# Performance work log

Measured on AMD Instinct MI355X. Metric: run time of the kernel, lower is better.

## Reference

```python
import jax, jax.numpy as jnp
import numpy as np

N_NODES = 50000
E0, E1 = 500000, 300000
D = 64  # node_embedding_size == h_feats == edge_embedding_sizes[i]


def _mlp(x, w0, b0, w1, b1, w2, b2):
    # Linear -> ReLU -> Linear -> ReLU -> Linear (nodes_in / edges_in stacks)
    h = jax.nn.relu(x @ w0 + b0)
    h = jax.nn.relu(h @ w1 + b1)
    return h @ w2 + b2


def setup_inputs() -> dict:
    key = jax.random.key(0)
    ks = jax.random.split(key, 32)

    def lin(k, fi, fo):
        return (jax.random.uniform(k, (fi, fo), jnp.float32) - 0.5) * (2.0 / np.sqrt(fi))

    z = lambda n: jnp.zeros((n,), jnp.float32)
    inp = {}
    inp['node_feats'] = jax.random.normal(ks[0], (N_NODES, 32), jnp.float32)
    inp['edge_feats0'] = jax.random.normal(ks[1], (E0, 16), jnp.float32)
    inp['edge_feats1'] = jax.random.normal(ks[2], (E1, 8), jnp.float32)
    # nodes_in MLP
    inp['n_w0'], inp['n_b0'] = lin(ks[3], 32, D), z(D)
    inp['n_w1'], inp['n_b1'] = lin(ks[4], D, D), z(D)
    inp['n_w2'], inp['n_b2'] = lin(ks[5], D, D), z(D)
    # edges_in MLP for edge type 0 (16 -> 64)
    inp['e0_w0'], inp['e0_b0'] = lin(ks[6], 16, D), z(D)
    inp['e0_w1'], inp['e0_b1'] = lin(ks[7], D, D), z(D)
    inp['e0_w2'], inp['e0_b2'] = lin(ks[8], D, D), z(D)
    # edges_in MLP for edge type 1 (8 -> 64)
    inp['e1_w0'], inp['e1_b0'] = lin(ks[9], 8, D), z(D)
    inp['e1_w1'], inp['e1_b1'] = lin(ks[10], D, D), z(D)
    inp['e1_w2'], inp['e1_b2'] = lin(ks[11], D, D), z(D)
    # GraphConv weights
    inp['c1_w'], inp['c1_b'] = lin(ks[12], D, D), z(D)
    inp['c2_w'], inp['c2_b'] = lin(ks[13], D, 1), z(1)
    # edge list (type-0 edges first, then type-1 edges)
    inp['src'] = jax.random.randint(ks[14], (E0 + E1,), 0, N_NODES, dtype=jnp.int32)
    inp['dst'] = jax.random.randint(ks[15], (E0 + E1,), 0, N_NODES, dtype=jnp.int32)
    return inp


def reference(node_feats, edge_feats0, edge_feats1,
              n_w0, n_b0, n_w1, n_b1, n_w2, n_b2,
              e0_w0, e0_b0, e0_w1, e0_b1, e0_w2, e0_b2,
              e1_w0, e1_b0, e1_w1, e1_b1, e1_w2, e1_b2,
              c1_w, c1_b, c2_w, c2_b, src, dst):
    n = node_feats.shape[0]
    # dense embedding stacks
    hn = _mlp(node_feats, n_w0, n_b0, n_w1, n_b1, n_w2, n_b2)          # [N, D]
    he = jnp.concatenate([
        _mlp(edge_feats0, e0_w0, e0_b0, e0_w1, e0_b1, e0_w2, e0_b2),
        _mlp(edge_feats1, e1_w0, e1_b0, e1_w1, e1_b1, e1_w2, e1_b2),
    ], axis=0)                                                          # [E, D]
    # GraphConv symmetric normalization (DGL norm='both'), degrees clamped to 1
    ones = jnp.ones(src.shape, jnp.float32)
    deg_out = jnp.maximum(jax.ops.segment_sum(ones, src, num_segments=n), 1.0)
    deg_in = jnp.maximum(jax.ops.segment_sum(ones, dst, num_segments=n), 1.0)
    norm_e = jax.lax.rsqrt(deg_out[src] * deg_in[dst])[:, None]        # [E, 1]
    # conv1: u_add_v message plus edge embedding, normalized sum aggregation
    msg = (hn[src] + hn[dst] + he) * norm_e                            # [E, D]
    agg1 = jax.ops.segment_sum(msg, dst, num_segments=n)               # [N, D]
    h1 = jax.nn.relu(agg1 @ c1_w + c1_b)                               # [N, D]
    # conv2: standard GraphConv to scalar output
    agg2 = jax.ops.segment_sum(h1[src] * norm_e, dst, num_segments=n)  # [N, D]
    return agg2 @ c2_w + c2_b                                          # [N, 1]
```

## Files before the change

### kernel.cpp

```cpp
#include <hip/hip_runtime.h>

#define N_NODES 50000
#define NE0 500000
#define NE1 300000
#define NE (NE0 + NE1)
#define DD 64

typedef __bf16 bf16x8 __attribute__((ext_vector_type(8)));
typedef float f32x4 __attribute__((ext_vector_type(4)));
typedef unsigned short u16x8 __attribute__((ext_vector_type(8)));

__device__ __forceinline__ ushort f2bf(float x) {
  union { __bf16 h; ushort u; } v;
  v.h = (__bf16)x;
  return v.u;
}
__device__ __forceinline__ float bf2f(ushort u) {
  union { unsigned u; float f; } v;
  v.u = ((unsigned)u) << 16;
  return v.f;
}

__device__ __forceinline__ int RP(const int* __restrict__ rowptr,
                                  const int* __restrict__ boff, int i) {
  return (i >= N_NODES) ? NE : rowptr[i] + boff[i >> 8];
}

__global__ void pack_k(const float* __restrict__ w00, const float* __restrict__ w01,
                       const float* __restrict__ w02, const float* __restrict__ w10,
                       const float* __restrict__ w11, const float* __restrict__ w12,
                       const float* __restrict__ w20, const float* __restrict__ w21,
                       const float* __restrict__ w22, ushort* __restrict__ pk) {
  int f = blockIdx.x, l = threadIdx.x;
  int t = f / 20, fl = f % 20;
  int layer, nt, ks;
  if (fl < 4) { layer = 0; nt = fl; ks = 0; }
  else if (fl < 12) { layer = 1; nt = (fl - 4) >> 1; ks = (fl - 4) & 1; }
  else { layer = 2; nt = (fl - 12) >> 1; ks = (fl - 12) & 1; }
  const float* Wt[3][3] = {{w00, w01, w02}, {w10, w11, w12}, {w20, w21, w22}};
  const int K0[3] = {16, 8, 32};
  const float* W = Wt[t][layer];
  int K = (layer == 0) ? K0[t] : 64;
  int g = l >> 4, c = l & 15;
  ushort o[8];
#pragma unroll
  for (int e = 0; e < 8; ++e) {
    int k = ks * 32 + g * 8 + e, n = nt * 16 + c;
    o[e] = f2bf((k < K) ? W[k * DD + n] : 0.f);
  }
  ushort4* d4 = (ushort4*)&pk[(size_t)f * 512 + l * 8];
  d4[0] = make_ushort4(o[0], o[1], o[2], o[3]);
  d4[1] = make_ushort4(o[4], o[5], o[6], o[7]);
}

__device__ __forceinline__ int block_scan_excl(int x, int tid, int* total) {
  int lane = tid & 63, w = tid >> 6;
  int incl = x;
#pragma unroll
  for (int d = 1; d < 64; d <<= 1) {
    int y = __shfl_up(incl, d);
    if (lane >= d) incl += y;
  }
  __shared__ int wsum[4];
  if (lane == 63) wsum[w] = incl;
  __syncthreads();
  int woff = 0;
  if (w > 0) woff = wsum[0];
  if (w > 1) woff += wsum[1];
  if (w > 2) woff += wsum[2];
  *total = wsum[0] + wsum[1] + wsum[2] + wsum[3];
  return woff + incl - x;
}

__global__ __launch_bounds__(256) void scan1_k(const int* __restrict__ cnt,
                                               int* __restrict__ rowptr,
                                               int* __restrict__ bsum) {
  int i = blockIdx.x * 256 + threadIdx.x;
  int x = (i < N_NODES) ? cnt[i] : 0;
  int tot;
  int ex = block_scan_excl(x, threadIdx.x, &tot);
  if (i < N_NODES) rowptr[i] = ex;
  if (threadIdx.x == 0) bsum[blockIdx.x] = tot;
}

__global__ __launch_bounds__(256) void scan2_k(const int* __restrict__ bsum,
                                               int* __restrict__ boff, int nb) {
  int i = threadIdx.x;
  int x = (i < nb) ? bsum[i] : 0;
  int tot;
  int ex = block_scan_excl(x, i, &tot);
  if (i < nb) boff[i] = ex;
}

__global__ void scatter_k(const int* __restrict__ src, const int* __restrict__ dst,
                          const int* __restrict__ rowptr, const int* __restrict__ boff,
                          int* __restrict__ fill, const int* __restrict__ cntO,
                          const int* __restrict__ cntI, int* __restrict__ ceid,
                          int* __restrict__ csrc, float* __restrict__ cnrm) {
  int e = blockIdx.x * 256 + threadIdx.x;
  if (e < NE) {
    int s = src[e], d = dst[e];
    int slot = RP(rowptr, boff, d) + atomicAdd(fill + d, 1);
    ceid[slot] = e;
    csrc[slot] = s;
    cnrm[slot] = rsqrtf((float)max(cntO[s], 1) * (float)max(cntI[d], 1));
  }
}

template <int FIN, bool NODE>
__device__ __forceinline__ void mlp_body(
    ushort (*__restrict__ A)[72], const float* __restrict__ xin,
    const ushort* __restrict__ pk, int pkb, const float* __restrict__ B0,
    const float* __restrict__ B1, const float* __restrict__ B2,
    ushort* __restrict__ msg, float* __restrict__ hn, int r0w, int nR,
    int ebase) {
  const int l = threadIdx.x & 63;
  const int g = l >> 4, c = l & 15;

  {
    int row = l >> 1, half = l & 1;
    int r = r0w + row;
    bool ok = r < nR;
    if (FIN == 32) {
      int cq = half * 16;
#pragma unroll
      for (int q = 0; q < 4; ++q) {
        float4 v = make_float4(0.f, 0.f, 0.f, 0.f);
        if (ok) v = *(const float4*)(xin + (size_t)r * 32 + cq + q * 4);
        *(ushort4*)&A[row][cq + q * 4] =
            make_ushort4(f2bf(v.x), f2bf(v.y), f2bf(v.z), f2bf(v.w));
      }
    } else if (FIN == 16) {
      int cq = half * 8;
#pragma unroll
      for (int q = 0; q < 2; ++q) {
        float4 v = make_float4(0.f, 0.f, 0.f, 0.f);
        if (ok) v = *(const float4*)(xin + (size_t)r * 16 + cq + q * 4);
        *(ushort4*)&A[row][cq + q * 4] =
            make_ushort4(f2bf(v.x), f2bf(v.y), f2bf(v.z), f2bf(v.w));
      }
    } else {
      int cq = half * 4;
      float4 v = make_float4(0.f, 0.f, 0.f, 0.f);
      if (ok) v = *(const float4*)(xin + (size_t)r * 8 + cq);
      *(ushort4*)&A[row][cq] =
          make_ushort4(f2bf(v.x), f2bf(v.y), f2bf(v.z), f2bf(v.w));
    }
  }
  asm volatile("s_waitcnt lgkmcnt(0)" ::: "memory");

  f32x4 acc[2][4];
#pragma unroll
  for (int nt = 0; nt < 4; ++nt) {
    float b = B0[nt * 16 + c];
    acc[0][nt] = f32x4{b, b, b, b};
    acc[1][nt] = acc[0][nt];
  }
  {
    bf16x8 a0 = {}, a1 = {};
    if (g * 8 < FIN) {
      a0 = *(const bf16x8*)&A[c][g * 8];
      a1 = *(const bf16x8*)&A[16 + c][g * 8];
    }
#pragma unroll
    for (int nt = 0; nt < 4; ++nt) {
      bf16x8 bb = *(const bf16x8*)&pk[(size_t)(pkb + nt) * 512 + l * 8];
      acc[0][nt] = __builtin_amdgcn_mfma_f32_16x16x32_bf16(a0, bb, acc[0][nt], 0, 0, 0);
      acc[1][nt] = __builtin_amdgcn_mfma_f32_16x16x32_bf16(a1, bb, acc[1][nt], 0, 0, 0);
    }
  }
#pragma unroll
  for (int t = 0; t < 2; ++t)
#pragma unroll
    for (int nt = 0; nt < 4; ++nt)
#pragma unroll
      for (int r = 0; r < 4; ++r)
        A[t * 16 + g * 4 + r][nt * 16 + c] = f2bf(fmaxf(acc[t][nt][r], 0.f));
  asm volatile("s_waitcnt lgkmcnt(0)" ::: "memory");

#pragma unroll
  for (int nt = 0; nt < 4; ++nt) {
    float b = B1[nt * 16 + c];
    acc[0][nt] = f32x4{b, b, b, b};
    acc[1][nt] = acc[0][nt];
  }
  {
    bf16x8 x00 = *(const bf16x8*)&A[c][g * 8];
    bf16x8 x01 = *(const bf16x8*)&A[c][32 + g * 8];
    bf16x8 x10 = *(const bf16x8*)&A[16 + c][g * 8];
    bf16x8 x11 = *(const bf16x8*)&A[16 + c][32 + g * 8];
#pragma unroll
    for (int nt = 0; nt < 4; ++nt) {
      bf16x8 bb0 = *(const bf16x8*)&pk[(size_t)(pkb + 4 + nt * 2) * 512 + l * 8];
      bf16x8 bb1 = *(const bf16x8*)&pk[(size_t)(pkb + 5 + nt * 2) * 512 + l * 8];
      acc[0][nt] = __builtin_amdgcn_mfma_f32_16x16x32_bf16(x00, bb0, acc[0][nt], 0, 0, 0);
      acc[0][nt] = __builtin_amdgcn_mfma_f32_16x16x32_bf16(x01, bb1, acc[0][nt], 0, 0, 0);
      acc[1][nt] = __builtin_amdgcn_mfma_f32_16x16x32_bf16(x10, bb0, acc[1][nt], 0, 0, 0);
      acc[1][nt] = __builtin_amdgcn_mfma_f32_16x16x32_bf16(x11, bb1, acc[1][nt], 0, 0, 0);
    }
  }
#pragma unroll
  for (int t = 0; t < 2; ++t)
#pragma unroll
    for (int nt = 0; nt < 4; ++nt)
#pragma unroll
      for (int r = 0; r < 4; ++r)
        A[t * 16 + g * 4 + r][nt * 16 + c] = f2bf(fmaxf(acc[t][nt][r], 0.f));
  asm volatile("s_waitcnt lgkmcnt(0)" ::: "memory");

#pragma unroll
  for (int nt = 0; nt < 4; ++nt) {
    float b = B2[nt * 16 + c];
    acc[0][nt] = f32x4{b, b, b, b};
    acc[1][nt] = acc[0][nt];
  }
  {
    bf16x8 x00 = *(const bf16x8*)&A[c][g * 8];
    bf16x8 x01 = *(const bf16x8*)&A[c][32 + g * 8];
    bf16x8 x10 = *(const bf16x8*)&A[16 + c][g * 8];
    bf16x8 x11 = *(const bf16x8*)&A[16 + c][32 + g * 8];
#pragma unroll
    for (int nt = 0; nt < 4; ++nt) {
      bf16x8 bb0 = *(const bf16x8*)&pk[(size_t)(pkb + 12 + nt * 2) * 512 + l * 8];
      bf16x8 bb1 = *(const bf16x8*)&pk[(size_t)(pkb + 13 + nt * 2) * 512 + l * 8];
      acc[0][nt] = __builtin_amdgcn_mfma_f32_16x16x32_bf16(x00, bb0, acc[0][nt], 0, 0, 0);
      acc[0][nt] = __builtin_amdgcn_mfma_f32_16x16x32_bf16(x01, bb1, acc[0][nt], 0, 0, 0);
      acc[1][nt] = __builtin_amdgcn_mfma_f32_16x16x32_bf16(x10, bb0, acc[1][nt], 0, 0, 0);
      acc[1][nt] = __builtin_amdgcn_mfma_f32_16x16x32_bf16(x11, bb1, acc[1][nt], 0, 0, 0);
    }
  }

  if (NODE) {
#pragma unroll
    for (int t = 0; t < 2; ++t)
#pragma unroll
      for (int r = 0; r < 4; ++r) {
        int n = r0w + t * 16 + g * 4 + r;
        if (n < nR) {
          float* hp = hn + (size_t)n * DD + c;
#pragma unroll
          for (int nt = 0; nt < 4; ++nt) hp[nt * 16] = acc[t][nt][r];
        }
      }
  } else {
#pragma unroll
    for (int t = 0; t < 2; ++t)
#pragma unroll
      for (int nt = 0; nt < 4; ++nt)
#pragma unroll
        for (int r = 0; r < 4; ++r)
          A[t * 16 + g * 4 + r][nt * 16 + c] = f2bf(acc[t][nt][r]);
    asm volatile("s_waitcnt lgkmcnt(0)" ::: "memory");
#pragma unroll
    for (int p = 0; p < 4; ++p) {
      int row = p * 8 + (l >> 3);
      int col8 = (l & 7) * 8;
      u16x8 v = *(const u16x8*)&A[row][col8];
      if (r0w + row < nR)
        *(u16x8*)(msg + (size_t)(ebase + r0w + row) * DD + col8) = v;
    }
  }
}

__global__ __launch_bounds__(256, 6) void giant_k(
    const float* __restrict__ nf, const float* __restrict__ ef0,
    const float* __restrict__ ef1, const ushort* __restrict__ pk,
    const float* __restrict__ nb0, const float* __restrict__ nb1,
    const float* __restrict__ nb2, const float* __restrict__ b00,
    const float* __restrict__ b01, const float* __restrict__ b02,
    const float* __restrict__ b10, const float* __restrict__ b11,
    const float* __restrict__ b12, const int* __restrict__ src,
    const int* __restrict__ dst, int* __restrict__ cntO,
    int* __restrict__ cntI, ushort* __restrict__ msg, float* __restrict__ hn,
    int NBc4, int NBn, int NB0v) {
  __shared__ __align__(16) ushort act[4][32][72];
  int bid = blockIdx.x, tid = threadIdx.x, wid = tid >> 6;
  if (bid < NBc4) {
    int t4 = (bid * 256 + tid) * 4;
    if (t4 < NE) {
      int4 s4 = *(const int4*)(src + t4);
      int4 d4 = *(const int4*)(dst + t4);
      atomicAdd(cntO + s4.x, 1);
      atomicAdd(cntO + s4.y, 1);
      atomicAdd(cntO + s4.z, 1);
      atomicAdd(cntO + s4.w, 1);
      atomicAdd(cntI + d4.x, 1);
      atomicAdd(cntI + d4.y, 1);
      atomicAdd(cntI + d4.z, 1);
      atomicAdd(cntI + d4.w, 1);
    }
    return;
  }
  ushort (*A)[72] = act[wid];
  bid -= NBc4;
  if (bid < NBn) {
    mlp_body<32, true>(A, nf, pk, 40, nb0, nb1, nb2, nullptr, hn,
                       bid * 128 + wid * 32, N_NODES, 0);
  } else if (bid < NBn + NB0v) {
    mlp_body<16, false>(A, ef0, pk, 0, b00, b01, b02, msg, nullptr,
                        (bid - NBn) * 128 + wid * 32, NE0, 0);
  } else {
    mlp_body<8, false>(A, ef1, pk, 20, b10, b11, b12, msg, nullptr,
                       (bid - NBn - NB0v) * 128 + wid * 32, NE1, NE0);
  }
}

__global__ __launch_bounds__(256) void gather_conv1_k(
    const int* __restrict__ rowptr, const int* __restrict__ boff,
    const int* __restrict__ ceid, const int* __restrict__ csrc,
    const float* __restrict__ cnrm, const ushort* __restrict__ msgb,
    const float* __restrict__ hn, const float* __restrict__ c1w,
    const float* __restrict__ c1b, const float* __restrict__ c2w,
    float* __restrict__ sbuf) {
  int w = threadIdx.x >> 6, l = threadIdx.x & 63;
  int g = l >> 4, c = l & 15;
  int n = blockIdx.x * 4 + w;
  if (n >= N_NODES) return;
  int r0 = RP(rowptr, boff, n), r1 = RP(rowptr, boff, n + 1);
  float a0 = 0.f, a1 = 0.f, a2 = 0.f, a3 = 0.f, sn = 0.f;
  for (int j0 = r0; j0 < r1; j0 += 8) {
    int ja = j0 + g, jb = j0 + 4 + g;
    bool va = ja < r1, vb = jb < r1;
    int jas = va ? ja : r0, jbs = vb ? jb : r0;
    int ea = ceid[jas], eb = ceid[jbs];
    int sa = csrc[jas], sb = csrc[jbs];
    float na = va ? cnrm[jas] : 0.f;
    float nb = vb ? cnrm[jbs] : 0.f;
    ushort4 ma = *(const ushort4*)(msgb + (size_t)ea * DD + c * 4);
    float4 hav = *(const float4*)(hn + (size_t)sa * DD + c * 4);
    ushort4 mb = *(const ushort4*)(msgb + (size_t)eb * DD + c * 4);
    float4 hbv = *(const float4*)(hn + (size_t)sb * DD + c * 4);
    a0 = fmaf(na, bf2f(ma.x) + hav.x, fmaf(nb, bf2f(mb.x) + hbv.x, a0));
    a1 = fmaf(na, bf2f(ma.y) + hav.y, fmaf(nb, bf2f(mb.y) + hbv.y, a1));
    a2 = fmaf(na, bf2f(ma.z) + hav.z, fmaf(nb, bf2f(mb.z) + hbv.z, a2));
    a3 = fmaf(na, bf2f(ma.w) + hav.w, fmaf(nb, bf2f(mb.w) + hbv.w, a3));
    sn += na + nb;
  }
  a0 += __shfl_xor(a0, 16); a0 += __shfl_xor(a0, 32);
  a1 += __shfl_xor(a1, 16); a1 += __shfl_xor(a1, 32);
  a2 += __shfl_xor(a2, 16); a2 += __shfl_xor(a2, 32);
  a3 += __shfl_xor(a3, 16); a3 += __shfl_xor(a3, 32);
  sn += __shfl_xor(sn, 16); sn += __shfl_xor(sn, 32);
  float4 hv = *(const float4*)(hn + (size_t)n * DD + c * 4);
  a0 = fmaf(sn, hv.x, a0);
  a1 = fmaf(sn, hv.y, a1);
  a2 = fmaf(sn, hv.z, a2);
  a3 = fmaf(sn, hv.w, a3);
  __shared__ float Asm[4][64];
  if (g == 0) *(float4*)&Asm[w][c * 4] = make_float4(a0, a1, a2, a3);
  float h = c1b[l];
#pragma unroll 8
  for (int k = 0; k < 64; ++k) h = fmaf(Asm[w][k], c1w[k * DD + l], h);
  h = fmaxf(h, 0.f);
  float v = h * c2w[l];
#pragma unroll
  for (int d = 32; d; d >>= 1) v += __shfl_xor(v, d);
  if (l == 0) sbuf[n] = v;
}

__global__ __launch_bounds__(256) void conv2_gather_k(
    const int* __restrict__ rowptr, const int* __restrict__ boff,
    const int* __restrict__ csrc, const float* __restrict__ cnrm,
    const float* __restrict__ sbuf, const float* __restrict__ c2b,
    float* __restrict__ out) {
  int n = blockIdx.x * 16 + (threadIdx.x >> 4);
  int c = threadIdx.x & 15;
  if (n >= N_NODES) return;
  int r0 = RP(rowptr, boff, n), r1 = RP(rowptr, boff, n + 1);
  float a = 0.f;
  for (int j = r0 + c; j < r1; j += 16) a = fmaf(cnrm[j], sbuf[csrc[j]], a);
  a += __shfl_xor(a, 1, 16);
  a += __shfl_xor(a, 2, 16);
  a += __shfl_xor(a, 4, 16);
  a += __shfl_xor(a, 8, 16);
  if (c == 0) out[n] = a + c2b[0];
}

extern "C" void kernel_launch(void* const* d_in, const int* in_sizes, int n_in,
                              void* d_out, int out_size, void* d_ws,
                              size_t ws_size, hipStream_t stream) {
  const float* nf   = (const float*)d_in[0];
  const float* ef0  = (const float*)d_in[1];
  const float* ef1  = (const float*)d_in[2];
  const float* n_w0 = (const float*)d_in[3];  const float* n_b0 = (const float*)d_in[4];
  const float* n_w1 = (const float*)d_in[5];  const float* n_b1 = (const float*)d_in[6];
  const float* n_w2 = (const float*)d_in[7];  const float* n_b2 = (const float*)d_in[8];
  const float* e0w0 = (const float*)d_in[9];  const float* e0b0 = (const float*)d_in[10];
  const float* e0w1 = (const float*)d_in[11]; const float* e0b1 = (const float*)d_in[12];
  const float* e0w2 = (const float*)d_in[13]; const float* e0b2 = (const float*)d_in[14];
  const float* e1w0 = (const float*)d_in[15]; const float* e1b0 = (const float*)d_in[16];
  const float* e1w1 = (const float*)d_in[17]; const float* e1b1 = (const float*)d_in[18];
  const float* e1w2 = (const float*)d_in[19]; const float* e1b2 = (const float*)d_in[20];
  const float* c1w  = (const float*)d_in[21]; const float* c1b  = (const float*)d_in[22];
  const float* c2w  = (const float*)d_in[23]; const float* c2b  = (const float*)d_in[24];
  const int* src = (const int*)d_in[25];
  const int* dst = (const int*)d_in[26];
  float* out = (float*)d_out;
  float* ws = (float*)d_ws;

  float*  hn     = ws;
  float*  sbuf   = ws + 3200000;
  int*    rowptr = (int*)(ws + 3250000);
  int*    cntI   = (int*)(ws + 3300008);
  int*    cntO   = (int*)(ws + 3350008);
  int*    fill   = (int*)(ws + 3400008);
  int*    bsum   = (int*)(ws + 3450008);
  int*    boff   = (int*)(ws + 3450264);
  int*    ceid   = (int*)(ws + 3460000);
  int*    csrc   = (int*)(ws + 4260000);
  float*  cnrm   = ws + 5060000;
  ushort* msg    = (ushort*)(ws + 5860000);
  ushort* pk     = (ushort*)(ws + 31500000);

  const int NB   = (N_NODES + 255) / 256;
  const int NBn  = (N_NODES + 127) / 128;
  const int NB0  = (NE0 + 127) / 128;
  const int NB1  = (NE1 + 127) / 128;
  const int NBc  = (NE + 255) / 256;
  const int NBc4 = (NE + 1023) / 1024;

  hipMemsetAsync(cntI, 0, (size_t)3 * N_NODES * sizeof(int), stream);
  pack_k<<<60, 64, 0, stream>>>(e0w0, e0w1, e0w2, e1w0, e1w1, e1w2, n_w0,
                                n_w1, n_w2, pk);
  giant_k<<<NBc4 + NBn + NB0 + NB1, 256, 0, stream>>>(
      nf, ef0, ef1, pk, n_b0, n_b1, n_b2, e0b0, e0b1, e0b2, e1b0, e1b1, e1b2,
      src, dst, cntO, cntI, msg, hn, NBc4, NBn, NB0);
  scan1_k<<<NB, 256, 0, stream>>>(cntI, rowptr, bsum);
  scan2_k<<<1, 256, 0, stream>>>(bsum, boff, NB);
  scatter_k<<<NBc, 256, 0, stream>>>(src, dst, rowptr, boff, fill, cntO, cntI,
                                     ceid, csrc, cnrm);
  gather_conv1_k<<<(N_NODES + 3) / 4, 256, 0, stream>>>(
      rowptr, boff, ceid, csrc, cnrm, msg, hn, c1w, c1b, c2w, sbuf);
  conv2_gather_k<<<(N_NODES + 15) / 16, 256, 0, stream>>>(
      rowptr, boff, csrc, cnrm, sbuf, c2b, out);
}
```

Measured before the change: 236.0 us.

## Interleave degree-count blocks with MLP blocks and deepen gather unroll

```diff
diff --git a/kernel.cpp b/kernel.cpp
--- a/kernel.cpp
+++ b/kernel.cpp
@@ -5,6 +5,7 @@
 #define NE1 300000
 #define NE (NE0 + NE1)
 #define DD 64
+#define ILV 9
 
 typedef __bf16 bf16x8 __attribute__((ext_vector_type(8)));
 typedef float f32x4 __attribute__((ext_vector_type(4)));
@@ -272,36 +273,40 @@
     const float* __restrict__ b12, const int* __restrict__ src,
     const int* __restrict__ dst, int* __restrict__ cntO,
     int* __restrict__ cntI, ushort* __restrict__ msg, float* __restrict__ hn,
-    int NBc4, int NBn, int NB0v) {
+    int NBc4, int NBn, int NB0v, int NB1v) {
   __shared__ __align__(16) ushort act[4][32][72];
   int bid = blockIdx.x, tid = threadIdx.x, wid = tid >> 6;
-  if (bid < NBc4) {
-    int t4 = (bid * 256 + tid) * 4;
-    if (t4 < NE) {
-      int4 s4 = *(const int4*)(src + t4);
-      int4 d4 = *(const int4*)(dst + t4);
-      atomicAdd(cntO + s4.x, 1);
-      atomicAdd(cntO + s4.y, 1);
-      atomicAdd(cntO + s4.z, 1);
-      atomicAdd(cntO + s4.w, 1);
-      atomicAdd(cntI + d4.x, 1);
-      atomicAdd(cntI + d4.y, 1);
-      atomicAdd(cntI + d4.z, 1);
-      atomicAdd(cntI + d4.w, 1);
+  int cnum = bid / ILV;
+  if (bid % ILV == ILV - 1) {
+    if (cnum < NBc4) {
+      int t4 = (cnum * 256 + tid) * 4;
+      if (t4 < NE) {
+        int4 s4 = *(const int4*)(src + t4);
+        int4 d4 = *(const int4*)(dst + t4);
+        atomicAdd(cntO + s4.x, 1);
+        atomicAdd(cntO + s4.y, 1);
+        atomicAdd(cntO + s4.z, 1);
+        atomicAdd(cntO + s4.w, 1);
+        atomicAdd(cntI + d4.x, 1);
+        atomicAdd(cntI + d4.y, 1);
+        atomicAdd(cntI + d4.z, 1);
+        atomicAdd(cntI + d4.w, 1);
+      }
     }
     return;
   }
+  int mb = bid - cnum;
+  if (mb >= NBn + NB0v + NB1v) return;
   ushort (*A)[72] = act[wid];
-  bid -= NBc4;
-  if (bid < NBn) {
+  if (mb < NBn) {
     mlp_body<32, true>(A, nf, pk, 40, nb0, nb1, nb2, nullptr, hn,
-                       bid * 128 + wid * 32, N_NODES, 0);
-  } else if (bid < NBn + NB0v) {
+                       mb * 128 + wid * 32, N_NODES, 0);
+  } else if (mb < NBn + NB0v) {
     mlp_body<16, false>(A, ef0, pk, 0, b00, b01, b02, msg, nullptr,
-                        (bid - NBn) * 128 + wid * 32, NE0, 0);
+                        (mb - NBn) * 128 + wid * 32, NE0, 0);
   } else {
     mlp_body<8, false>(A, ef1, pk, 20, b10, b11, b12, msg, nullptr,
-                       (bid - NBn - NB0v) * 128 + wid * 32, NE1, NE0);
+                       (mb - NBn - NB0v) * 128 + wid * 32, NE1, NE0);
   }
 }
 
@@ -318,23 +323,22 @@
   if (n >= N_NODES) return;
   int r0 = RP(rowptr, boff, n), r1 = RP(rowptr, boff, n + 1);
   float a0 = 0.f, a1 = 0.f, a2 = 0.f, a3 = 0.f, sn = 0.f;
-  for (int j0 = r0; j0 < r1; j0 += 8) {
-    int ja = j0 + g, jb = j0 + 4 + g;
-    bool va = ja < r1, vb = jb < r1;
-    int jas = va ? ja : r0, jbs = vb ? jb : r0;
-    int ea = ceid[jas], eb = ceid[jbs];
-    int sa = csrc[jas], sb = csrc[jbs];
-    float na = va ? cnrm[jas] : 0.f;
-    float nb = vb ? cnrm[jbs] : 0.f;
-    ushort4 ma = *(const ushort4*)(msgb + (size_t)ea * DD + c * 4);
-    float4 hav = *(const float4*)(hn + (size_t)sa * DD + c * 4);
-    ushort4 mb = *(const ushort4*)(msgb + (size_t)eb * DD + c * 4);
-    float4 hbv = *(const float4*)(hn + (size_t)sb * DD + c * 4);
-    a0 = fmaf(na, bf2f(ma.x) + hav.x, fmaf(nb, bf2f(mb.x) + hbv.x, a0));
-    a1 = fmaf(na, bf2f(ma.y) + hav.y, fmaf(nb, bf2f(mb.y) + hbv.y, a1));
-    a2 = fmaf(na, bf2f(ma.z) + hav.z, fmaf(nb, bf2f(mb.z) + hbv.z, a2));
-    a3 = fmaf(na, bf2f(ma.w) + hav.w, fmaf(nb, bf2f(mb.w) + hbv.w, a3));
-    sn += na + nb;
+  for (int j0 = r0; j0 < r1; j0 += 16) {
+#pragma unroll
+    for (int u = 0; u < 4; ++u) {
+      int j = j0 + u * 4 + g;
+      bool v = j < r1;
+      int js = v ? j : r0;
+      int e = ceid[js], s = csrc[js];
+      float nm = v ? cnrm[js] : 0.f;
+      ushort4 m = *(const ushort4*)(msgb + (size_t)e * DD + c * 4);
+      float4 h = *(const float4*)(hn + (size_t)s * DD + c * 4);
+      a0 = fmaf(nm, bf2f(m.x) + h.x, a0);
+      a1 = fmaf(nm, bf2f(m.y) + h.y, a1);
+      a2 = fmaf(nm, bf2f(m.z) + h.z, a2);
+      a3 = fmaf(nm, bf2f(m.w) + h.w, a3);
+      sn += nm;
+    }
   }
   a0 += __shfl_xor(a0, 16); a0 += __shfl_xor(a0, 32);
   a1 += __shfl_xor(a1, 16); a1 += __shfl_xor(a1, 32);
@@ -419,12 +423,16 @@
   const int NBc  = (NE + 255) / 256;
   const int NBc4 = (NE + 1023) / 1024;
 
+  const int NMLP = NBn + NB0 + NB1;
+  int T = NMLP + NBc4;
+  while (T / ILV < NBc4 || T - T / ILV < NMLP) ++T;
+
   hipMemsetAsync(cntI, 0, (size_t)3 * N_NODES * sizeof(int), stream);
   pack_k<<<60, 64, 0, stream>>>(e0w0, e0w1, e0w2, e1w0, e1w1, e1w2, n_w0,
                                 n_w1, n_w2, pk);
-  giant_k<<<NBc4 + NBn + NB0 + NB1, 256, 0, stream>>>(
+  giant_k<<<T, 256, 0, stream>>>(
       nf, ef0, ef1, pk, n_b0, n_b1, n_b2, e0b0, e0b1, e0b2, e1b0, e1b1, e1b2,
-      src, dst, cntO, cntI, msg, hn, NBc4, NBn, NB0);
+      src, dst, cntO, cntI, msg, hn, NBc4, NBn, NB0, NB1);
   scan1_k<<<NB, 256, 0, stream>>>(cntI, rowptr, bsum);
   scan2_k<<<1, 256, 0, stream>>>(bsum, boff, NB);
   scatter_k<<<NBc, 256, 0, stream>>>(src, dst, rowptr, boff, fill, cntO, cntI,
```

New measurement: 218.4 us. 1.08x faster.
